# Optimization experiments

Measured on AMD Instinct MI355X. Metric: run time of the kernel, lower is better.

Reference implementation:

```python
import jax, jax.numpy as jnp
import numpy as np


def setup_inputs() -> dict:
    key = jax.random.key(0)
    k1, k2 = jax.random.split(key)
    B, C, H, W = 4, 64, 256, 512
    right_input = jax.random.normal(k1, (B, C, H, W), dtype=jnp.float32)
    disparity_samples = jax.random.uniform(k2, (B, 1, H, W), dtype=jnp.float32)
    return {"right_input": right_input, "disparity_samples": disparity_samples}


def reference(right_input, disparity_samples):
    B, C, H, W = right_input.shape
    dt = right_input.dtype
    # left pixel x-coordinates along width, broadcast over B,1,H
    left_y = jnp.arange(W, dtype=dt).reshape(1, 1, 1, W)
    right_y = left_y + disparity_samples                      # [B,1,H,W]
    ry_a = jnp.floor(right_y)
    ry_b = ry_a + 1.0
    wa = ry_b - right_y                                       # [B,1,H,W]
    wb = right_y - ry_a
    idx_a = jnp.clip(ry_a, 0, W - 1).astype(jnp.int32)
    idx_b = jnp.clip(ry_b, 0, W - 1).astype(jnp.int32)
    # broadcast indices across channels and gather along width (dim=3)
    idx_a = jnp.broadcast_to(idx_a, (B, C, H, W))
    idx_b = jnp.broadcast_to(idx_b, (B, C, H, W))
    feat_a = jnp.take_along_axis(right_input, idx_a, axis=3)
    feat_b = jnp.take_along_axis(right_input, idx_b, axis=3)
    warped = wa * feat_a + wb * feat_b                        # weights broadcast over C
    # zero out samples whose (unclamped) coordinate fell outside [0, W-1]
    oob = (right_y < 0).astype(dt) + (right_y > (W - 1)).astype(dt)
    return (1.0 - oob) * warped
```

## Files before the change

### kernel.cpp

```cpp
#include <hip/hip_runtime.h>

constexpr int B = 4;
constexpr int C = 64;
constexpr int H = 256;
constexpr int W = 512;
constexpr int CH_PER_BLOCK = 16;
constexpr int ROWS_PER_ITER = 2;

__global__ __launch_bounds__(256) void spatial_warp_kernel(
    const float* __restrict__ input,
    const float* __restrict__ disp,
    float* __restrict__ out)
{
    __shared__ float s_row[ROWS_PER_ITER * W];
    __shared__ float s_disp[W];

    const int t = threadIdx.x;
    const int cg = blockIdx.x % (C / CH_PER_BLOCK);
    int rest = blockIdx.x / (C / CH_PER_BLOCK);
    const int h = rest % H;
    const int b = rest / H;
    const int c_base = cg * CH_PER_BLOCK;

    const long long pix_base = ((long long)b * H + h) * W;
    if (t < W / 4) {
        reinterpret_cast<float4*>(s_disp)[t] =
            reinterpret_cast<const float4*>(disp + pix_base)[t];
    }
    __syncthreads();

    const int r     = t >> 7;
    const int lane7 = t & 127;

    float wa4[4], wb4[4], msk[4];
    int   ia4[4], ib4[4];
#pragma unroll
    for (int i = 0; i < 4; ++i) {
        const int w  = lane7 + 128 * i;
        const float d  = s_disp[w];
        const float ry = (float)w + d;
        const float ra = floorf(ry);
        const float rb = ra + 1.0f;
        wa4[i] = rb - ry;
        wb4[i] = ry - ra;
        ia4[i] = (int)fminf(fmaxf(ra, 0.0f), (float)(W - 1));
        ib4[i] = (int)fminf(fmaxf(rb, 0.0f), (float)(W - 1));
        msk[i] = (ry >= 0.0f && ry <= (float)(W - 1)) ? 1.0f : 0.0f;
    }

    const int lds_base = r * W;
#pragma unroll 2
    for (int cc = 0; cc < CH_PER_BLOCK / ROWS_PER_ITER; ++cc) {
        const int c_mine = c_base + cc * ROWS_PER_ITER + r;
        const float* rowg = input + (((long long)b * C + c_mine) * H + h) * (long long)W;
        const float4 v = reinterpret_cast<const float4*>(rowg)[lane7];
        __syncthreads();
        reinterpret_cast<float4*>(s_row + lds_base)[lane7] = v;
        __syncthreads();

        float* outg = out + (((long long)b * C + c_mine) * H + h) * (long long)W;
#pragma unroll
        for (int i = 0; i < 4; ++i) {
            const int w = lane7 + 128 * i;
            const float fa = s_row[lds_base + ia4[i]];
            const float fb = s_row[lds_base + ib4[i]];
            outg[w] = msk[i] * (wa4[i] * fa + wb4[i] * fb);
        }
    }
}

extern "C" void kernel_launch(void* const* d_in, const int* in_sizes, int n_in,
                              void* d_out, int out_size, void* d_ws, size_t ws_size,
                              hipStream_t stream) {
    const float* input = (const float*)d_in[0];
    const float* disp  = (const float*)d_in[1];
    float* outp = (float*)d_out;

    const int grid = B * H * (C / CH_PER_BLOCK);
    spatial_warp_kernel<<<grid, 256, 0, stream>>>(input, disp, outp);
}
```

Baseline: 235.9 us.

## Give each wavefront private LDS rows and drop block-wide barriers

Each wavefront now handles its own four channels, staging every channel row into a wave-private double-buffered LDS slot. This removes the block-wide __syncthreads that were needed because all waves shared rows. The next row's global loads are issued before the current row is computed, the disparity row is read directly from global memory instead of through LDS, and the mask is folded into the weights so the edge case becomes a single adjacent pair. It relies on lockstep execution within a wavefront plus an explicit lgkmcnt wait instead of a barrier. There is a small redundant leftover pointer computation.

```diff
diff --git a/kernel.cpp b/kernel.cpp
--- a/kernel.cpp
+++ b/kernel.cpp
@@ -5,66 +5,80 @@
 constexpr int H = 256;
 constexpr int W = 512;
 constexpr int CH_PER_BLOCK = 16;
-constexpr int ROWS_PER_ITER = 2;
+constexpr int WAVES = 4;
+constexpr int CH_PER_WAVE = CH_PER_BLOCK / WAVES;
 
 __global__ __launch_bounds__(256) void spatial_warp_kernel(
     const float* __restrict__ input,
     const float* __restrict__ disp,
     float* __restrict__ out)
 {
-    __shared__ float s_row[ROWS_PER_ITER * W];
-    __shared__ float s_disp[W];
+    __shared__ float s_rows[WAVES][2][W];
 
-    const int t = threadIdx.x;
+    const int t    = threadIdx.x;
+    const int lane = t & 63;
+    const int wid  = t >> 6;
+
     const int cg = blockIdx.x % (C / CH_PER_BLOCK);
-    int rest = blockIdx.x / (C / CH_PER_BLOCK);
-    const int h = rest % H;
-    const int b = rest / H;
-    const int c_base = cg * CH_PER_BLOCK;
+    int rest     = blockIdx.x / (C / CH_PER_BLOCK);
+    const int h  = rest % H;
+    const int b  = rest / H;
+    const int c0 = cg * CH_PER_BLOCK + wid * CH_PER_WAVE;
 
-    const long long pix_base = ((long long)b * H + h) * W;
-    if (t < W / 4) {
-        reinterpret_cast<float4*>(s_disp)[t] =
-            reinterpret_cast<const float4*>(disp + pix_base)[t];
-    }
-    __syncthreads();
+    const long long pix = ((long long)b * H + h) * (long long)W;
 
-    const int r     = t >> 7;
-    const int lane7 = t & 127;
-
-    float wa4[4], wb4[4], msk[4];
-    int   ia4[4], ib4[4];
+    float waf[8], wbf[8];
+    int   addr0[8];
+    const float* drow = disp + pix;
 #pragma unroll
-    for (int i = 0; i < 4; ++i) {
-        const int w  = lane7 + 128 * i;
-        const float d  = s_disp[w];
+    for (int j = 0; j < 8; ++j) {
+        const int w   = lane + 64 * j;
+        const float d  = drow[w];
         const float ry = (float)w + d;
         const float ra = floorf(ry);
-        const float rb = ra + 1.0f;
-        wa4[i] = rb - ry;
-        wb4[i] = ry - ra;
-        ia4[i] = (int)fminf(fmaxf(ra, 0.0f), (float)(W - 1));
-        ib4[i] = (int)fminf(fmaxf(rb, 0.0f), (float)(W - 1));
-        msk[i] = (ry >= 0.0f && ry <= (float)(W - 1)) ? 1.0f : 0.0f;
+        const float wa = ra + 1.0f - ry;
+        const float wb = ry - ra;
+        const float msk = (ry >= 0.0f && ry <= (float)(W - 1)) ? 1.0f : 0.0f;
+        const float iaf = fminf(fmaxf(ra, 0.0f), (float)(W - 1));
+        const int   ia  = (int)iaf;
+        const bool  hi  = (ia >= W - 1);
+        const int   i0  = hi ? (W - 2) : ia;
+        waf[j]   = hi ? 0.0f : msk * wa;
+        wbf[j]   = hi ? msk  : msk * wb;
+        addr0[j] = i0 * 4;
     }
 
-    const int lds_base = r * W;
-#pragma unroll 2
-    for (int cc = 0; cc < CH_PER_BLOCK / ROWS_PER_ITER; ++cc) {
-        const int c_mine = c_base + cc * ROWS_PER_ITER + r;
-        const float* rowg = input + (((long long)b * C + c_mine) * H + h) * (long long)W;
-        const float4 v = reinterpret_cast<const float4*>(rowg)[lane7];
-        __syncthreads();
-        reinterpret_cast<float4*>(s_row + lds_base)[lane7] = v;
-        __syncthreads();
+    const long long chStride = (long long)H * W;
+    const float* grow = input + ((long long)(b * C + c0)) * chStride + pix % ((long long)H * W)
+                        ;
+    grow = input + (((long long)b * C + c0) * H + h) * (long long)W;
+    float* orow = out + (((long long)b * C + c0) * H + h) * (long long)W;
 
-        float* outg = out + (((long long)b * C + c_mine) * H + h) * (long long)W;
+    float4 v0 = reinterpret_cast<const float4*>(grow)[lane];
+    float4 v1 = reinterpret_cast<const float4*>(grow)[64 + lane];
+
 #pragma unroll
-        for (int i = 0; i < 4; ++i) {
-            const int w = lane7 + 128 * i;
-            const float fa = s_row[lds_base + ia4[i]];
-            const float fb = s_row[lds_base + ib4[i]];
-            outg[w] = msk[i] * (wa4[i] * fa + wb4[i] * fb);
+    for (int cc = 0; cc < CH_PER_WAVE; ++cc) {
+        float* buf = &s_rows[wid][cc & 1][0];
+        reinterpret_cast<float4*>(buf)[lane]      = v0;
+        reinterpret_cast<float4*>(buf)[64 + lane] = v1;
+
+        if (cc + 1 < CH_PER_WAVE) {
+            const float* gnext = grow + (long long)(cc + 1) * chStride;
+            v0 = reinterpret_cast<const float4*>(gnext)[lane];
+            v1 = reinterpret_cast<const float4*>(gnext)[64 + lane];
+        }
+
+        asm volatile("s_waitcnt lgkmcnt(0)" ::: "memory");
+
+        float* op = orow + (long long)cc * chStride;
+#pragma unroll
+        for (int j = 0; j < 8; ++j) {
+            const float fa = *reinterpret_cast<const float*>(
+                reinterpret_cast<const char*>(buf) + addr0[j]);
+            const float fb = *reinterpret_cast<const float*>(
+                reinterpret_cast<const char*>(buf) + addr0[j] + 4);
+            op[lane + 64 * j] = waf[j] * fa + wbf[j] * fb;
         }
     }
 }
```

Result: no change. 240.4 us (+1.9%).
